# Kernel optimization log

Measured on AMD Instinct MI355X. Metric: run time of the kernel, lower is better.

## Reference

```python
import jax, jax.numpy as jnp
import numpy as np

STRIDE = 1
PAD = 1
DIL = 1


def setup_inputs() -> dict:
    key = jax.random.key(0)
    k1, k2, k3, k4 = jax.random.split(key, 4)
    N, Cin, H, W = 4, 256, 64, 64
    Cout, kh, kw = 256, 3, 3
    inputs = jax.random.normal(k1, (N, Cin, H, W), jnp.float32)
    filter = jax.random.normal(k2, (Cout, Cin, kh, kw), jnp.float32) * 0.05
    # offsets in pixels (y,x interleaved per tap), typical magnitude O(1)
    offset = jax.random.normal(k3, (N, 2 * kh * kw, H, W), jnp.float32)
    # modulation mask in [0,1) (post-sigmoid in real nets)
    mask = jax.random.uniform(k4, (N, kh * kw, H, W), jnp.float32)
    return {"inputs": inputs, "filter": filter, "offset": offset, "mask": mask}


def _dcn_forward(inputs, filt, offset, mask):
    N, C, H, W = inputs.shape
    Cout, _, kh, kw = filt.shape
    K = kh * kw
    Ho = (H + 2 * PAD - DIL * (kh - 1) - 1) // STRIDE + 1
    Wo = (W + 2 * PAD - DIL * (kw - 1) - 1) // STRIDE + 1

    # base sampling grid per kernel tap: [K, Ho, Wo]
    ki, kj = jnp.meshgrid(jnp.arange(kh), jnp.arange(kw), indexing='ij')
    ki = ki.reshape(K, 1, 1)
    kj = kj.reshape(K, 1, 1)
    base_y = (jnp.arange(Ho)[None, :, None] * STRIDE - PAD + ki * DIL).astype(jnp.float32)
    base_x = (jnp.arange(Wo)[None, None, :] * STRIDE - PAD + kj * DIL).astype(jnp.float32)

    # offset channels: per tap k, channel 2k = dy, channel 2k+1 = dx
    off = offset.reshape(N, K, 2, Ho, Wo)
    y = base_y[None] + off[:, :, 0]  # [N, K, Ho, Wo]
    x = base_x[None] + off[:, :, 1]

    y0 = jnp.floor(y)
    x0 = jnp.floor(x)
    ly = y - y0  # fractional parts, [N, K, Ho, Wo]
    lx = x - x0
    y0i = y0.astype(jnp.int32)
    x0i = x0.astype(jnp.int32)

    def gather(img, yy, xx):
        # img [C,H,W]; yy,xx [K,Ho,Wo] int; zero outside bounds
        valid = (yy >= 0) & (yy < H) & (xx >= 0) & (xx < W)
        yc = jnp.clip(yy, 0, H - 1)
        xc = jnp.clip(xx, 0, W - 1)
        return img[:, yc, xc] * valid.astype(img.dtype)  # [C,K,Ho,Wo]

    def sample_one(img, y0i, x0i, ly, lx):
        v00 = gather(img, y0i, x0i)
        v01 = gather(img, y0i, x0i + 1)
        v10 = gather(img, y0i + 1, x0i)
        v11 = gather(img, y0i + 1, x0i + 1)
        return (v00 * (1 - ly) * (1 - lx) + v01 * (1 - ly) * lx
                + v10 * ly * (1 - lx) + v11 * ly * lx)

    # bilinear-sampled, modulated im2col columns: [N, C, K, Ho, Wo]
    col = jax.vmap(sample_one)(inputs, y0i, x0i, ly, lx)
    col = col * mask.reshape(N, 1, K, Ho, Wo)

    # grouped conv with num_groups=1: plain GEMM over (C, K)
    out = jnp.einsum('ock,nckhw->nohw', filt.reshape(Cout, C, K), col)
    return out


def reference(inputs, filter, offset, mask):
    return _dcn_forward(inputs, filter, offset, mask)
```

## Files before the change

### kernel.cpp

```cpp
#include <hip/hip_runtime.h>
#include <stdint.h>

typedef __attribute__((ext_vector_type(2))) float f32x2;
typedef __attribute__((ext_vector_type(4))) float f32x4;
typedef __attribute__((ext_vector_type(8))) short bf16x8;

static constexpr int N_ = 4, C_ = 256, HW_ = 4096;
static constexpr int CO_ = 256, KTAP = 9;
static constexpr int NSTEP = 72;
static constexpr int A_PLANE = 16 * 64 * 16;

static constexpr size_t NHWC_BYTES = (size_t)N_ * HW_ * C_ * 2;
static constexpr size_t ABF_OFF    = NHWC_BYTES;
static constexpr size_t ABF_BYTES  = (size_t)NSTEP * A_PLANE;

__device__ inline unsigned f2bf(float f) {
  unsigned u = __builtin_bit_cast(unsigned, f);
  unsigned r = u + 0x7FFFu + ((u >> 16) & 1u);
  return r >> 16;
}
__device__ inline float asf(unsigned u) { return __builtin_bit_cast(float, u); }

__global__ __launch_bounds__(256) void k_prep(const float* __restrict__ in,
                                              const float* __restrict__ filt,
                                              unsigned short* __restrict__ nhwc,
                                              unsigned short* __restrict__ abf2) {
  int b = blockIdx.x;
  int t = threadIdx.x;
  if (b < 1024) {
    __shared__ float tile[64][65];
    int n = b >> 8, cg = (b >> 6) & 3, hwg = b & 63;
    int c0 = cg * 64, hw0 = hwg * 64;
    int col = t & 63, r0 = t >> 6;
#pragma unroll
    for (int i = 0; i < 16; ++i) {
      int row = r0 + i * 4;
      tile[row][col] = in[(size_t)(n * C_ + c0 + row) * HW_ + hw0 + col];
    }
    __syncthreads();
    int pr = t >> 2, cc0 = (t & 3) * 16;
    unsigned us[8];
#pragma unroll
    for (int i = 0; i < 8; ++i) {
      unsigned lo = f2bf(tile[cc0 + 2 * i][pr]);
      unsigned hi = f2bf(tile[cc0 + 2 * i + 1][pr]);
      us[i] = lo | (hi << 16);
    }
    unsigned* dst = (unsigned*)(nhwc + (size_t)(n * HW_ + hw0 + pr) * C_ + c0 + cc0);
    ((uint4*)dst)[0] = make_uint4(us[0], us[1], us[2], us[3]);
    ((uint4*)dst)[1] = make_uint4(us[4], us[5], us[6], us[7]);
  } else {
    int gid = (b - 1024) * 256 + t;
    int o = gid >> 8, c = gid & 255;
    const float* f = filt + (size_t)(o * C_ + c) * KTAP;
    int rb = o >> 4;
    int lane = ((c >> 3) & 3) * 16 + (o & 15);
    int j = c & 7;
#pragma unroll
    for (int tap = 0; tap < KTAP; ++tap) {
      int s = tap * 8 + (c >> 5);
      abf2[((size_t)(s * 16 + rb) * 64 + lane) * 8 + j] = (unsigned short)f2bf(f[tap]);
    }
  }
}

__device__ __forceinline__ f32x2 unpk(unsigned u) {
  return (f32x2){asf(u << 16), asf(u & 0xffff0000u)};
}

__device__ __forceinline__ uint4 comb8(const uint4& g0, const uint4& g1,
                                       const uint4& g2, const uint4& g3, f32x4 w) {
  f32x2 r0 = w.x * unpk(g0.x) + w.y * unpk(g1.x) + w.z * unpk(g2.x) + w.w * unpk(g3.x);
  f32x2 r1 = w.x * unpk(g0.y) + w.y * unpk(g1.y) + w.z * unpk(g2.y) + w.w * unpk(g3.y);
  f32x2 r2 = w.x * unpk(g0.z) + w.y * unpk(g1.z) + w.z * unpk(g2.z) + w.w * unpk(g3.z);
  f32x2 r3 = w.x * unpk(g0.w) + w.y * unpk(g1.w) + w.z * unpk(g2.w) + w.w * unpk(g3.w);
  unsigned o0, o1, o2, o3;
  asm("v_cvt_pk_bf16_f32 %0, %1, %2" : "=v"(o0) : "v"(r0.x), "v"(r0.y));
  asm("v_cvt_pk_bf16_f32 %0, %1, %2" : "=v"(o1) : "v"(r1.x), "v"(r1.y));
  asm("v_cvt_pk_bf16_f32 %0, %1, %2" : "=v"(o2) : "v"(r2.x), "v"(r2.y));
  asm("v_cvt_pk_bf16_f32 %0, %1, %2" : "=v"(o3) : "v"(r3.x), "v"(r3.y));
  return make_uint4(o0, o1, o2, o3);
}

#define MFMA_BF16 __builtin_amdgcn_mfma_f32_16x16x32_bf16

__global__ __launch_bounds__(512, 2) void k_dcn(const unsigned short* __restrict__ nhwc,
                                                const unsigned short* __restrict__ abf2,
                                                const float* __restrict__ offs,
                                                const float* __restrict__ msk,
                                                float* __restrict__ out) {
  __shared__ __align__(16) unsigned short Bl[2][16384];
  __shared__ float recW[KTAP * 64 * 4];
  __shared__ unsigned recA[KTAP * 64 * 4];

  int bid = blockIdx.x;
  int b = ((bid & 7) << 5) | (bid >> 3);
  int n = b >> 6;
  int ho = b & 63;
  int hw0 = ho << 6;
  int t = threadIdx.x;

  for (int r = t; r < 576; r += 512) {
    int pl = r / 9;
    int tap = r - pl * 9;
    int hw = hw0 + pl;
    float dy = offs[(size_t)(n * 18 + 2 * tap) * HW_ + hw];
    float dx = offs[(size_t)(n * 18 + 2 * tap + 1) * HW_ + hw];
    float mk = msk[(size_t)(n * 9 + tap) * HW_ + hw];
    float y = (float)(ho - 1 + tap / 3) + dy;
    float x = (float)(pl - 1 + tap % 3) + dx;
    float fy = floorf(y), fx = floorf(x);
    float ly = y - fy, lx = x - fx;
    int y0 = (int)fy, x0 = (int)fx;
    int y1 = y0 + 1, x1 = x0 + 1;
    float vy0 = (y0 >= 0 && y0 < 64) ? 1.f : 0.f;
    float vy1 = (y1 >= 0 && y1 < 64) ? 1.f : 0.f;
    float vx0 = (x0 >= 0 && x0 < 64) ? 1.f : 0.f;
    float vx1 = (x1 >= 0 && x1 < 64) ? 1.f : 0.f;
    int y0c = min(max(y0, 0), 63), y1c = min(max(y1, 0), 63);
    int x0c = min(max(x0, 0), 63), x1c = min(max(x1, 0), 63);
    int base = (tap * 64 + pl) * 4;
    recW[base + 0] = (1.f - ly) * (1.f - lx) * mk * vy0 * vx0;
    recW[base + 1] = (1.f - ly) * lx * mk * vy0 * vx1;
    recW[base + 2] = ly * (1.f - lx) * mk * vy1 * vx0;
    recW[base + 3] = ly * lx * mk * vy1 * vx1;
    recA[base + 0] = (unsigned)((y0c * 64 + x0c) * 512);
    recA[base + 1] = (unsigned)((y0c * 64 + x1c) * 512);
    recA[base + 2] = (unsigned)((y1c * 64 + x0c) * 512);
    recA[base + 3] = (unsigned)((y1c * 64 + x1c) * 512);
  }
  __syncthreads();

  int lane = t & 63, wv = t >> 6;
  int px = t >> 3, cq = t & 7;
  unsigned cq16 = (unsigned)(cq * 16);
  const char* nb = (const char*)nhwc + (size_t)n * HW_ * C_ * 2;
  const int wchunk = (cq & 3) * 1024 + px * 16;
  const int sj0 = (cq >> 2) * 4096;

  const char* aoff = (const char*)abf2 + ((wv * 2) * 64 + lane) * 16;
  int kq = lane >> 4, pxl = lane & 15;
  const int bo0 = kq * 1024 + (0 * 16 + pxl) * 16;
  const int bo1 = kq * 1024 + (1 * 16 + pxl) * 16;
  const int bo2 = kq * 1024 + (2 * 16 + pxl) * 16;
  const int bo3 = kq * 1024 + (3 * 16 + pxl) * 16;

  f32x4 acc[2][4];
#pragma unroll
  for (int mi = 0; mi < 2; ++mi)
#pragma unroll
    for (int ni = 0; ni < 4; ++ni) acc[mi][ni] = (f32x4){0.f, 0.f, 0.f, 0.f};

  bf16x8 afc0, afc1, afn0, afn1;

  {
    f32x4 w0 = *(const f32x4*)&recW[px * 4];
    uint4 ra = *(const uint4*)&recA[px * 4];
    uint4 g0[4], g1[4], g2[4], g3[4];
#pragma unroll
    for (int j = 0; j < 4; ++j) {
      unsigned o_ = (unsigned)(j * 128) + cq16;
      g0[j] = *(const uint4*)(nb + ra.x + o_);
      g1[j] = *(const uint4*)(nb + ra.y + o_);
      g2[j] = *(const uint4*)(nb + ra.z + o_);
      g3[j] = *(const uint4*)(nb + ra.w + o_);
    }
    char* wb = (char*)&Bl[0][0] + sj0 + wchunk;
#pragma unroll
    for (int j = 0; j < 4; ++j)
      *(uint4*)(wb + j * 8192) = comb8(g0[j], g1[j], g2[j], g3[j], w0);
  }
  afc0 = *(const bf16x8*)(aoff);
  afc1 = *(const bf16x8*)(aoff + 1024);
  __syncthreads();

  for (int tap = 0; tap < KTAP; ++tap) {
    const int rd = (tap & 1) << 15;
    const int wr = rd ^ (1 << 15);

    uint4 g0[4], g1[4], g2[4], g3[4];
    f32x4 wN;
    if (tap < KTAP - 1) {
      wN = *(const f32x4*)&recW[((tap + 1) * 64 + px) * 4];
      uint4 ra = *(const uint4*)&recA[((tap + 1) * 64 + px) * 4];
#pragma unroll
      for (int j = 0; j < 4; ++j) {
        unsigned o_ = (unsigned)(j * 128) + cq16;
        g0[j] = *(const uint4*)(nb + ra.x + o_);
        g1[j] = *(const uint4*)(nb + ra.y + o_);
        g2[j] = *(const uint4*)(nb + ra.z + o_);
        g3[j] = *(const uint4*)(nb + ra.w + o_);
      }
    }
    __builtin_amdgcn_sched_barrier(0);

#pragma unroll
    for (int s8 = 0; s8 < 8; ++s8) {
      int gs1 = tap * 8 + s8 + 1;
      if (gs1 >= NSTEP) gs1 = NSTEP - 1;
      afn0 = *(const bf16x8*)(aoff + (size_t)gs1 * A_PLANE);
      afn1 = *(const bf16x8*)(aoff + (size_t)gs1 * A_PLANE + 1024);
      const char* bb = (const char*)&Bl[0][0] + rd + s8 * 4096;
      bf16x8 b0 = *(const bf16x8*)(bb + bo0);
      bf16x8 b1 = *(const bf16x8*)(bb + bo1);
      bf16x8 b2 = *(const bf16x8*)(bb + bo2);
      bf16x8 b3 = *(const bf16x8*)(bb + bo3);
      __builtin_amdgcn_s_setprio(1);
      acc[0][0] = MFMA_BF16(afc0, b0, acc[0][0], 0, 0, 0);
      acc[1][0] = MFMA_BF16(afc1, b0, acc[1][0], 0, 0, 0);
      acc[0][1] = MFMA_BF16(afc0, b1, acc[0][1], 0, 0, 0);
      acc[1][1] = MFMA_BF16(afc1, b1, acc[1][1], 0, 0, 0);
      acc[0][2] = MFMA_BF16(afc0, b2, acc[0][2], 0, 0, 0);
      acc[1][2] = MFMA_BF16(afc1, b2, acc[1][2], 0, 0, 0);
      acc[0][3] = MFMA_BF16(afc0, b3, acc[0][3], 0, 0, 0);
      acc[1][3] = MFMA_BF16(afc1, b3, acc[1][3], 0, 0, 0);
      __builtin_amdgcn_s_setprio(0);
      afc0 = afn0;
      afc1 = afn1;
    }

    if (tap < KTAP - 1) {
      char* wb = (char*)&Bl[0][0] + wr + sj0 + wchunk;
#pragma unroll
      for (int j = 0; j < 4; ++j)
        *(uint4*)(wb + j * 8192) = comb8(g0[j], g1[j], g2[j], g3[j], wN);
      asm volatile("s_waitcnt lgkmcnt(0)" ::: "memory");
    }
    __builtin_amdgcn_sched_barrier(0);
    __builtin_amdgcn_s_barrier();
    asm volatile("" ::: "memory");
  }

  float* ob = out + (size_t)n * CO_ * HW_ + hw0;
#pragma unroll
  for (int mi = 0; mi < 2; ++mi)
#pragma unroll
    for (int ni = 0; ni < 4; ++ni)
#pragma unroll
      for (int jj = 0; jj < 4; ++jj) {
        int o = wv * 32 + mi * 16 + (lane >> 4) * 4 + jj;
        int hw = ni * 16 + (lane & 15);
        ob[(size_t)o * HW_ + hw] = acc[mi][ni][jj];
      }
}

extern "C" void kernel_launch(void* const* d_in, const int* in_sizes, int n_in,
                              void* d_out, int out_size, void* d_ws, size_t ws_size,
                              hipStream_t stream) {
  const float* inp  = (const float*)d_in[0];
  const float* filt = (const float*)d_in[1];
  const float* offs = (const float*)d_in[2];
  const float* msk  = (const float*)d_in[3];
  float* out = (float*)d_out;
  if (ws_size < ABF_OFF + ABF_BYTES) return;
  unsigned short* nhwc = (unsigned short*)d_ws;
  unsigned short* abf2 = (unsigned short*)((char*)d_ws + ABF_OFF);

  k_prep<<<1280, 256, 0, stream>>>(inp, filt, nhwc, abf2);
  k_dcn<<<256, 512, 0, stream>>>(nhwc, abf2, offs, msk, out);
}
```

Before: 49.59 us.

## Double block to 1024 threads, split pixel tile across wave pairs, deepen A prefetch

```diff
diff --git a/kernel.cpp b/kernel.cpp
--- a/kernel.cpp
+++ b/kernel.cpp
@@ -84,11 +84,30 @@
 
 #define MFMA_BF16 __builtin_amdgcn_mfma_f32_16x16x32_bf16
 
-__global__ __launch_bounds__(512, 2) void k_dcn(const unsigned short* __restrict__ nhwc,
-                                                const unsigned short* __restrict__ abf2,
-                                                const float* __restrict__ offs,
-                                                const float* __restrict__ msk,
-                                                float* __restrict__ out) {
+#define GSTEP(S8)                                                              \
+  do {                                                                         \
+    int g4_ = tap * 8 + (S8) + 4;                                              \
+    if (g4_ >= NSTEP) g4_ = NSTEP - 1;                                         \
+    const char* bb_ = (const char*)&Bl[0][0] + rd + (S8) * 4096;               \
+    bf16x8 b0_ = *(const bf16x8*)(bb_ + bo0);                                  \
+    bf16x8 b1_ = *(const bf16x8*)(bb_ + bo1);                                  \
+    bf16x8 a0_ = aR[(S8) & 3][0];                                              \
+    bf16x8 a1_ = aR[(S8) & 3][1];                                              \
+    aR[(S8) & 3][0] = *(const bf16x8*)(aoffb + (size_t)g4_ * A_PLANE);         \
+    aR[(S8) & 3][1] = *(const bf16x8*)(aoffb + (size_t)g4_ * A_PLANE + 1024);  \
+    __builtin_amdgcn_s_setprio(1);                                             \
+    acc[0][0] = MFMA_BF16(a0_, b0_, acc[0][0], 0, 0, 0);                       \
+    acc[1][0] = MFMA_BF16(a1_, b0_, acc[1][0], 0, 0, 0);                       \
+    acc[0][1] = MFMA_BF16(a0_, b1_, acc[0][1], 0, 0, 0);                       \
+    acc[1][1] = MFMA_BF16(a1_, b1_, acc[1][1], 0, 0, 0);                       \
+    __builtin_amdgcn_s_setprio(0);                                             \
+  } while (0)
+
+__global__ __launch_bounds__(1024, 4) void k_dcn(const unsigned short* __restrict__ nhwc,
+                                                 const unsigned short* __restrict__ abf2,
+                                                 const float* __restrict__ offs,
+                                                 const float* __restrict__ msk,
+                                                 float* __restrict__ out) {
   __shared__ __align__(16) unsigned short Bl[2][16384];
   __shared__ float recW[KTAP * 64 * 4];
   __shared__ unsigned recA[KTAP * 64 * 4];
@@ -100,7 +119,8 @@
   int hw0 = ho << 6;
   int t = threadIdx.x;
 
-  for (int r = t; r < 576; r += 512) {
+  if (t < 576) {
+    int r = t;
     int pl = r / 9;
     int tap = r - pl * 9;
     int hw = hw0 + pl;
@@ -132,114 +152,98 @@
   __syncthreads();
 
   int lane = t & 63, wv = t >> 6;
-  int px = t >> 3, cq = t & 7;
-  unsigned cq16 = (unsigned)(cq * 16);
+  int ig = wv >> 1, jg = wv & 1;
+
+  int px = t >> 4, cg = t & 15;
+  unsigned cgo = (unsigned)(cg * 16);
   const char* nb = (const char*)nhwc + (size_t)n * HW_ * C_ * 2;
-  const int wchunk = (cq & 3) * 1024 + px * 16;
-  const int sj0 = (cq >> 2) * 4096;
-
-  const char* aoff = (const char*)abf2 + ((wv * 2) * 64 + lane) * 16;
+  const int wchunk = (cg & 3) * 1024 + px * 16;
+  const int sj0 = (cg >> 2) * 4096;
+
+  const char* aoffb = (const char*)abf2 + ((ig * 2) * 64 + lane) * 16;
   int kq = lane >> 4, pxl = lane & 15;
-  const int bo0 = kq * 1024 + (0 * 16 + pxl) * 16;
-  const int bo1 = kq * 1024 + (1 * 16 + pxl) * 16;
-  const int bo2 = kq * 1024 + (2 * 16 + pxl) * 16;
-  const int bo3 = kq * 1024 + (3 * 16 + pxl) * 16;
-
-  f32x4 acc[2][4];
+  const int bo0 = kq * 1024 + (jg * 32 + 0 * 16 + pxl) * 16;
+  const int bo1 = kq * 1024 + (jg * 32 + 1 * 16 + pxl) * 16;
+
+  f32x4 acc[2][2];
 #pragma unroll
   for (int mi = 0; mi < 2; ++mi)
 #pragma unroll
-    for (int ni = 0; ni < 4; ++ni) acc[mi][ni] = (f32x4){0.f, 0.f, 0.f, 0.f};
-
-  bf16x8 afc0, afc1, afn0, afn1;
+    for (int ni = 0; ni < 2; ++ni) acc[mi][ni] = (f32x4){0.f, 0.f, 0.f, 0.f};
+
+  bf16x8 aR[4][2];
 
   {
     f32x4 w0 = *(const f32x4*)&recW[px * 4];
     uint4 ra = *(const uint4*)&recA[px * 4];
-    uint4 g0[4], g1[4], g2[4], g3[4];
-#pragma unroll
-    for (int j = 0; j < 4; ++j) {
-      unsigned o_ = (unsigned)(j * 128) + cq16;
-      g0[j] = *(const uint4*)(nb + ra.x + o_);
-      g1[j] = *(const uint4*)(nb + ra.y + o_);
-      g2[j] = *(const uint4*)(nb + ra.z + o_);
-      g3[j] = *(const uint4*)(nb + ra.w + o_);
-    }
-    char* wb = (char*)&Bl[0][0] + sj0 + wchunk;
-#pragma unroll
-    for (int j = 0; j < 4; ++j)
-      *(uint4*)(wb + j * 8192) = comb8(g0[j], g1[j], g2[j], g3[j], w0);
-  }
-  afc0 = *(const bf16x8*)(aoff);
-  afc1 = *(const bf16x8*)(aoff + 1024);
+    uint4 g0 = *(const uint4*)(nb + ra.x + cgo);
+    uint4 g1 = *(const uint4*)(nb + ra.y + cgo);
+    uint4 g2 = *(const uint4*)(nb + ra.z + cgo);
+    uint4 g3 = *(const uint4*)(nb + ra.w + cgo);
+    *(uint4*)((char*)&Bl[0][0] + sj0 + wchunk) = comb8(g0, g1, g2, g3, w0);
+    g0 = *(const uint4*)(nb + ra.x + cgo + 256);
+    g1 = *(const uint4*)(nb + ra.y + cgo + 256);
+    g2 = *(const uint4*)(nb + ra.z + cgo + 256);
+    g3 = *(const uint4*)(nb + ra.w + cgo + 256);
+    *(uint4*)((char*)&Bl[0][0] + sj0 + 16384 + wchunk) = comb8(g0, g1, g2, g3, w0);
+  }
+#pragma unroll
+  for (int k = 0; k < 4; ++k) {
+    aR[k][0] = *(const bf16x8*)(aoffb + (size_t)k * A_PLANE);
+    aR[k][1] = *(const bf16x8*)(aoffb + (size_t)k * A_PLANE + 1024);
+  }
   __syncthreads();
 
   for (int tap = 0; tap < KTAP; ++tap) {
     const int rd = (tap & 1) << 15;
     const int wr = rd ^ (1 << 15);
-
-    uint4 g0[4], g1[4], g2[4], g3[4];
+    const bool more = tap < KTAP - 1;
+
+    uint4 ga0, ga1, ga2, ga3;
     f32x4 wN;
-    if (tap < KTAP - 1) {
+    uint4 raN;
+    if (more) {
       wN = *(const f32x4*)&recW[((tap + 1) * 64 + px) * 4];
-      uint4 ra = *(const uint4*)&recA[((tap + 1) * 64 + px) * 4];
-#pragma unroll
-      for (int j = 0; j < 4; ++j) {
-        unsigned o_ = (unsigned)(j * 128) + cq16;
-        g0[j] = *(const uint4*)(nb + ra.x + o_);
-        g1[j] = *(const uint4*)(nb + ra.y + o_);
-        g2[j] = *(const uint4*)(nb + ra.z + o_);
-        g3[j] = *(const uint4*)(nb + ra.w + o_);
-      }
+      raN = *(const uint4*)&recA[((tap + 1) * 64 + px) * 4];
+      ga0 = *(const uint4*)(nb + raN.x + cgo);
+      ga1 = *(const uint4*)(nb + raN.y + cgo);
+      ga2 = *(const uint4*)(nb + raN.z + cgo);
+      ga3 = *(const uint4*)(nb + raN.w + cgo);
     }
     __builtin_amdgcn_sched_barrier(0);
 
-#pragma unroll
-    for (int s8 = 0; s8 < 8; ++s8) {
-      int gs1 = tap * 8 + s8 + 1;
-      if (gs1 >= NSTEP) gs1 = NSTEP - 1;
-      afn0 = *(const bf16x8*)(aoff + (size_t)gs1 * A_PLANE);
-      afn1 = *(const bf16x8*)(aoff + (size_t)gs1 * A_PLANE + 1024);
-      const char* bb = (const char*)&Bl[0][0] + rd + s8 * 4096;
-      bf16x8 b0 = *(const bf16x8*)(bb + bo0);
-      bf16x8 b1 = *(const bf16x8*)(bb + bo1);
-      bf16x8 b2 = *(const bf16x8*)(bb + bo2);
-      bf16x8 b3 = *(const bf16x8*)(bb + bo3);
-      __builtin_amdgcn_s_setprio(1);
-      acc[0][0] = MFMA_BF16(afc0, b0, acc[0][0], 0, 0, 0);
-      acc[1][0] = MFMA_BF16(afc1, b0, acc[1][0], 0, 0, 0);
-      acc[0][1] = MFMA_BF16(afc0, b1, acc[0][1], 0, 0, 0);
-      acc[1][1] = MFMA_BF16(afc1, b1, acc[1][1], 0, 0, 0);
-      acc[0][2] = MFMA_BF16(afc0, b2, acc[0][2], 0, 0, 0);
-      acc[1][2] = MFMA_BF16(afc1, b2, acc[1][2], 0, 0, 0);
-      acc[0][3] = MFMA_BF16(afc0, b3, acc[0][3], 0, 0, 0);
-      acc[1][3] = MFMA_BF16(afc1, b3, acc[1][3], 0, 0, 0);
-      __builtin_amdgcn_s_setprio(0);
-      afc0 = afn0;
-      afc1 = afn1;
-    }
-
-    if (tap < KTAP - 1) {
-      char* wb = (char*)&Bl[0][0] + wr + sj0 + wchunk;
-#pragma unroll
-      for (int j = 0; j < 4; ++j)
-        *(uint4*)(wb + j * 8192) = comb8(g0[j], g1[j], g2[j], g3[j], wN);
-      asm volatile("s_waitcnt lgkmcnt(0)" ::: "memory");
-    }
+    GSTEP(0); GSTEP(1); GSTEP(2); GSTEP(3);
+
+    if (more) {
+      *(uint4*)((char*)&Bl[0][0] + wr + sj0 + wchunk) = comb8(ga0, ga1, ga2, ga3, wN);
+      ga0 = *(const uint4*)(nb + raN.x + cgo + 256);
+      ga1 = *(const uint4*)(nb + raN.y + cgo + 256);
+      ga2 = *(const uint4*)(nb + raN.z + cgo + 256);
+      ga3 = *(const uint4*)(nb + raN.w + cgo + 256);
+    }
+    __builtin_amdgcn_sched_barrier(0);
+
+    GSTEP(4); GSTEP(5); GSTEP(6); GSTEP(7);
+
+    if (more) {
+      *(uint4*)((char*)&Bl[0][0] + wr + sj0 + 16384 + wchunk) =
+          comb8(ga0, ga1, ga2, ga3, wN);
+    }
+    asm volatile("s_waitcnt lgkmcnt(0)" ::: "memory");
     __builtin_amdgcn_sched_barrier(0);
     __builtin_amdgcn_s_barrier();
     asm volatile("" ::: "memory");
   }
 
-  float* ob = out + (size_t)n * CO_ * HW_ + hw0;
+  float* ob = out + (size_t)n * CO_ * HW_ + hw0 + jg * 32;
 #pragma unroll
   for (int mi = 0; mi < 2; ++mi)
 #pragma unroll
-    for (int ni = 0; ni < 4; ++ni)
+    for (int ni = 0; ni < 2; ++ni)
 #pragma unroll
       for (int jj = 0; jj < 4; ++jj) {
-        int o = wv * 32 + mi * 16 + (lane >> 4) * 4 + jj;
-        int hw = ni * 16 + (lane & 15);
+        int o = ig * 32 + mi * 16 + kq * 4 + jj;
+        int hw = ni * 16 + pxl;
         ob[(size_t)o * HW_ + hw] = acc[mi][ni][jj];
       }
 }
@@ -257,5 +261,5 @@
   unsigned short* abf2 = (unsigned short*)((char*)d_ws + ABF_OFF);
 
   k_prep<<<1280, 256, 0, stream>>>(inp, filt, nhwc, abf2);
-  k_dcn<<<256, 512, 0, stream>>>(nhwc, abf2, offs, msk, out);
-}
+  k_dcn<<<256, 1024, 0, stream>>>(nhwc, abf2, offs, msk, out);
+}
```

Result: no change. 49.57 us (-0.0%).

## Split DCN kernel into producer gather waves and consumer MFMA waves

Applied to the files above, without the earlier changes.

```diff
diff --git a/kernel.cpp b/kernel.cpp
--- a/kernel.cpp
+++ b/kernel.cpp
@@ -84,11 +84,36 @@
 
 #define MFMA_BF16 __builtin_amdgcn_mfma_f32_16x16x32_bf16
 
-__global__ __launch_bounds__(512, 2) void k_dcn(const unsigned short* __restrict__ nhwc,
-                                                const unsigned short* __restrict__ abf2,
-                                                const float* __restrict__ offs,
-                                                const float* __restrict__ msk,
-                                                float* __restrict__ out) {
+#define GSTEP(S8)                                                              \
+  do {                                                                         \
+    int g4_ = tap * 8 + (S8) + 4;                                              \
+    if (g4_ >= NSTEP) g4_ = NSTEP - 1;                                         \
+    const char* bb_ = (const char*)&Bl[0][0] + rd + (S8) * 4096;               \
+    bf16x8 b0_ = *(const bf16x8*)(bb_ + bo0);                                  \
+    bf16x8 b1_ = *(const bf16x8*)(bb_ + bo1);                                  \
+    bf16x8 b2_ = *(const bf16x8*)(bb_ + bo2);                                  \
+    bf16x8 b3_ = *(const bf16x8*)(bb_ + bo3);                                  \
+    bf16x8 a0_ = aR[(S8) & 3][0];                                              \
+    bf16x8 a1_ = aR[(S8) & 3][1];                                              \
+    aR[(S8) & 3][0] = *(const bf16x8*)(aoffb + (size_t)g4_ * A_PLANE);         \
+    aR[(S8) & 3][1] = *(const bf16x8*)(aoffb + (size_t)g4_ * A_PLANE + 1024);  \
+    __builtin_amdgcn_s_setprio(1);                                             \
+    acc[0][0] = MFMA_BF16(a0_, b0_, acc[0][0], 0, 0, 0);                       \
+    acc[1][0] = MFMA_BF16(a1_, b0_, acc[1][0], 0, 0, 0);                       \
+    acc[0][1] = MFMA_BF16(a0_, b1_, acc[0][1], 0, 0, 0);                       \
+    acc[1][1] = MFMA_BF16(a1_, b1_, acc[1][1], 0, 0, 0);                       \
+    acc[0][2] = MFMA_BF16(a0_, b2_, acc[0][2], 0, 0, 0);                       \
+    acc[1][2] = MFMA_BF16(a1_, b2_, acc[1][2], 0, 0, 0);                       \
+    acc[0][3] = MFMA_BF16(a0_, b3_, acc[0][3], 0, 0, 0);                       \
+    acc[1][3] = MFMA_BF16(a1_, b3_, acc[1][3], 0, 0, 0);                       \
+    __builtin_amdgcn_s_setprio(0);                                             \
+  } while (0)
+
+__global__ __launch_bounds__(1024, 4) void k_dcn(const unsigned short* __restrict__ nhwc,
+                                                 const unsigned short* __restrict__ abf2,
+                                                 const float* __restrict__ offs,
+                                                 const float* __restrict__ msk,
+                                                 float* __restrict__ out) {
   __shared__ __align__(16) unsigned short Bl[2][16384];
   __shared__ float recW[KTAP * 64 * 4];
   __shared__ unsigned recA[KTAP * 64 * 4];
@@ -100,7 +125,8 @@
   int hw0 = ho << 6;
   int t = threadIdx.x;
 
-  for (int r = t; r < 576; r += 512) {
+  if (t < 576) {
+    int r = t;
     int pl = r / 9;
     int tap = r - pl * 9;
     int hw = hw0 + pl;
@@ -132,57 +158,64 @@
   __syncthreads();
 
   int lane = t & 63, wv = t >> 6;
-  int px = t >> 3, cq = t & 7;
-  unsigned cq16 = (unsigned)(cq * 16);
-  const char* nb = (const char*)nhwc + (size_t)n * HW_ * C_ * 2;
-  const int wchunk = (cq & 3) * 1024 + px * 16;
-  const int sj0 = (cq >> 2) * 4096;
-
-  const char* aoff = (const char*)abf2 + ((wv * 2) * 64 + lane) * 16;
-  int kq = lane >> 4, pxl = lane & 15;
-  const int bo0 = kq * 1024 + (0 * 16 + pxl) * 16;
-  const int bo1 = kq * 1024 + (1 * 16 + pxl) * 16;
-  const int bo2 = kq * 1024 + (2 * 16 + pxl) * 16;
-  const int bo3 = kq * 1024 + (3 * 16 + pxl) * 16;
-
-  f32x4 acc[2][4];
-#pragma unroll
-  for (int mi = 0; mi < 2; ++mi)
-#pragma unroll
-    for (int ni = 0; ni < 4; ++ni) acc[mi][ni] = (f32x4){0.f, 0.f, 0.f, 0.f};
-
-  bf16x8 afc0, afc1, afn0, afn1;
-
-  {
-    f32x4 w0 = *(const f32x4*)&recW[px * 4];
-    uint4 ra = *(const uint4*)&recA[px * 4];
-    uint4 g0[4], g1[4], g2[4], g3[4];
-#pragma unroll
-    for (int j = 0; j < 4; ++j) {
-      unsigned o_ = (unsigned)(j * 128) + cq16;
-      g0[j] = *(const uint4*)(nb + ra.x + o_);
-      g1[j] = *(const uint4*)(nb + ra.y + o_);
-      g2[j] = *(const uint4*)(nb + ra.z + o_);
-      g3[j] = *(const uint4*)(nb + ra.w + o_);
-    }
-    char* wb = (char*)&Bl[0][0] + sj0 + wchunk;
-#pragma unroll
-    for (int j = 0; j < 4; ++j)
-      *(uint4*)(wb + j * 8192) = comb8(g0[j], g1[j], g2[j], g3[j], w0);
-  }
-  afc0 = *(const bf16x8*)(aoff);
-  afc1 = *(const bf16x8*)(aoff + 1024);
-  __syncthreads();
-
-  for (int tap = 0; tap < KTAP; ++tap) {
-    const int rd = (tap & 1) << 15;
-    const int wr = rd ^ (1 << 15);
-
-    uint4 g0[4], g1[4], g2[4], g3[4];
-    f32x4 wN;
-    if (tap < KTAP - 1) {
-      wN = *(const f32x4*)&recW[((tap + 1) * 64 + px) * 4];
-      uint4 ra = *(const uint4*)&recA[((tap + 1) * 64 + px) * 4];
+  bool cons = wv < 8;
+
+  if (cons) {
+    const char* aoffb = (const char*)abf2 + ((wv * 2) * 64 + lane) * 16;
+    int kq = lane >> 4, pxl = lane & 15;
+    const int bo0 = kq * 1024 + (0 * 16 + pxl) * 16;
+    const int bo1 = kq * 1024 + (1 * 16 + pxl) * 16;
+    const int bo2 = kq * 1024 + (2 * 16 + pxl) * 16;
+    const int bo3 = kq * 1024 + (3 * 16 + pxl) * 16;
+
+    f32x4 acc[2][4];
+#pragma unroll
+    for (int mi = 0; mi < 2; ++mi)
+#pragma unroll
+      for (int ni = 0; ni < 4; ++ni) acc[mi][ni] = (f32x4){0.f, 0.f, 0.f, 0.f};
+
+    bf16x8 aR[4][2];
+#pragma unroll
+    for (int k = 0; k < 4; ++k) {
+      aR[k][0] = *(const bf16x8*)(aoffb + (size_t)k * A_PLANE);
+      aR[k][1] = *(const bf16x8*)(aoffb + (size_t)k * A_PLANE + 1024);
+    }
+    asm volatile("" ::: "memory");
+    __builtin_amdgcn_s_barrier();
+    asm volatile("" ::: "memory");
+
+    for (int tap = 0; tap < KTAP; ++tap) {
+      const int rd = (tap & 1) << 15;
+      GSTEP(0); GSTEP(1); GSTEP(2); GSTEP(3);
+      GSTEP(4); GSTEP(5); GSTEP(6); GSTEP(7);
+      asm volatile("" ::: "memory");
+      __builtin_amdgcn_s_barrier();
+      asm volatile("" ::: "memory");
+    }
+
+    float* ob = out + (size_t)n * CO_ * HW_ + hw0;
+#pragma unroll
+    for (int mi = 0; mi < 2; ++mi)
+#pragma unroll
+      for (int ni = 0; ni < 4; ++ni)
+#pragma unroll
+        for (int jj = 0; jj < 4; ++jj) {
+          int o = wv * 32 + mi * 16 + kq * 4 + jj;
+          int hw = ni * 16 + pxl;
+          ob[(size_t)o * HW_ + hw] = acc[mi][ni][jj];
+        }
+  } else {
+    int p = t - 512;
+    int px = p >> 3, cq = p & 7;
+    unsigned cq16 = (unsigned)(cq * 16);
+    const char* nb = (const char*)nhwc + (size_t)n * HW_ * C_ * 2;
+    const int wchunk = (cq & 3) * 1024 + px * 16;
+    const int sj0 = (cq >> 2) * 4096;
+
+    {
+      f32x4 w0 = *(const f32x4*)&recW[px * 4];
+      uint4 ra = *(const uint4*)&recA[px * 4];
+      uint4 g0[4], g1[4], g2[4], g3[4];
 #pragma unroll
       for (int j = 0; j < 4; ++j) {
         unsigned o_ = (unsigned)(j * 128) + cq16;
@@ -191,57 +224,41 @@
         g2[j] = *(const uint4*)(nb + ra.z + o_);
         g3[j] = *(const uint4*)(nb + ra.w + o_);
       }
-    }
-    __builtin_amdgcn_sched_barrier(0);
-
-#pragma unroll
-    for (int s8 = 0; s8 < 8; ++s8) {
-      int gs1 = tap * 8 + s8 + 1;
-      if (gs1 >= NSTEP) gs1 = NSTEP - 1;
-      afn0 = *(const bf16x8*)(aoff + (size_t)gs1 * A_PLANE);
-      afn1 = *(const bf16x8*)(aoff + (size_t)gs1 * A_PLANE + 1024);
-      const char* bb = (const char*)&Bl[0][0] + rd + s8 * 4096;
-      bf16x8 b0 = *(const bf16x8*)(bb + bo0);
-      bf16x8 b1 = *(const bf16x8*)(bb + bo1);
-      bf16x8 b2 = *(const bf16x8*)(bb + bo2);
-      bf16x8 b3 = *(const bf16x8*)(bb + bo3);
-      __builtin_amdgcn_s_setprio(1);
-      acc[0][0] = MFMA_BF16(afc0, b0, acc[0][0], 0, 0, 0);
-      acc[1][0] = MFMA_BF16(afc1, b0, acc[1][0], 0, 0, 0);
-      acc[0][1] = MFMA_BF16(afc0, b1, acc[0][1], 0, 0, 0);
-      acc[1][1] = MFMA_BF16(afc1, b1, acc[1][1], 0, 0, 0);
-      acc[0][2] = MFMA_BF16(afc0, b2, acc[0][2], 0, 0, 0);
-      acc[1][2] = MFMA_BF16(afc1, b2, acc[1][2], 0, 0, 0);
-      acc[0][3] = MFMA_BF16(afc0, b3, acc[0][3], 0, 0, 0);
-      acc[1][3] = MFMA_BF16(afc1, b3, acc[1][3], 0, 0, 0);
-      __builtin_amdgcn_s_setprio(0);
-      afc0 = afn0;
-      afc1 = afn1;
-    }
-
-    if (tap < KTAP - 1) {
-      char* wb = (char*)&Bl[0][0] + wr + sj0 + wchunk;
+      char* wb = (char*)&Bl[0][0] + sj0 + wchunk;
 #pragma unroll
       for (int j = 0; j < 4; ++j)
-        *(uint4*)(wb + j * 8192) = comb8(g0[j], g1[j], g2[j], g3[j], wN);
+        *(uint4*)(wb + j * 8192) = comb8(g0[j], g1[j], g2[j], g3[j], w0);
       asm volatile("s_waitcnt lgkmcnt(0)" ::: "memory");
     }
-    __builtin_amdgcn_sched_barrier(0);
+    asm volatile("" ::: "memory");
     __builtin_amdgcn_s_barrier();
     asm volatile("" ::: "memory");
+
+    for (int tap = 0; tap < KTAP; ++tap) {
+      const int wr = ((tap & 1) ^ 1) << 15;
+      if (tap < KTAP - 1) {
+        f32x4 wN = *(const f32x4*)&recW[((tap + 1) * 64 + px) * 4];
+        uint4 raN = *(const uint4*)&recA[((tap + 1) * 64 + px) * 4];
+        uint4 g0[4], g1[4], g2[4], g3[4];
+#pragma unroll
+        for (int j = 0; j < 4; ++j) {
+          unsigned o_ = (unsigned)(j * 128) + cq16;
+          g0[j] = *(const uint4*)(nb + raN.x + o_);
+          g1[j] = *(const uint4*)(nb + raN.y + o_);
+          g2[j] = *(const uint4*)(nb + raN.z + o_);
+          g3[j] = *(const uint4*)(nb + raN.w + o_);
+        }
+        char* wb = (char*)&Bl[0][0] + wr + sj0 + wchunk;
+#pragma unroll
+        for (int j = 0; j < 4; ++j)
+          *(uint4*)(wb + j * 8192) = comb8(g0[j], g1[j], g2[j], g3[j], wN);
+        asm volatile("s_waitcnt lgkmcnt(0)" ::: "memory");
+      }
+      asm volatile("" ::: "memory");
+      __builtin_amdgcn_s_barrier();
+      asm volatile("" ::: "memory");
+    }
   }
-
-  float* ob = out + (size_t)n * CO_ * HW_ + hw0;
-#pragma unroll
-  for (int mi = 0; mi < 2; ++mi)
-#pragma unroll
-    for (int ni = 0; ni < 4; ++ni)
-#pragma unroll
-      for (int jj = 0; jj < 4; ++jj) {
-        int o = wv * 32 + mi * 16 + (lane >> 4) * 4 + jj;
-        int hw = ni * 16 + (lane & 15);
-        ob[(size_t)o * HW_ + hw] = acc[mi][ni][jj];
-      }
 }
 
 extern "C" void kernel_launch(void* const* d_in, const int* in_sizes, int n_in,
@@ -257,5 +274,5 @@
   unsigned short* abf2 = (unsigned short*)((char*)d_ws + ABF_OFF);
 
   k_prep<<<1280, 256, 0, stream>>>(inp, filt, nhwc, abf2);
-  k_dcn<<<256, 512, 0, stream>>>(nhwc, abf2, offs, msk, out);
-}
+  k_dcn<<<256, 1024, 0, stream>>>(nhwc, abf2, offs, msk, out);
+}
```

After: 45.85 us. 1.08x faster.
